# Performance work log

Measured on AMD Instinct MI355X. Metric: run time of the kernel, lower is better.

## Reference

```python
import jax, jax.numpy as jnp
import numpy as np

COMMITMENT_COST = 0.25


def setup_inputs() -> dict:
    key = jax.random.key(0)
    k1, k2 = jax.random.split(key)
    x = jax.random.normal(k1, (65536, 256), dtype=jnp.float32)
    codebook = jax.random.normal(k2, (1024, 256), dtype=jnp.float32)
    return {"x": x, "codebook": codebook}


def reference(x, codebook):
    # Flatten to [N, D] (already 2D here).
    flat = x.reshape(-1, codebook.shape[1])
    # Squared euclidean distances [N, K]; argmin matches torch.cdist argmin.
    x2 = jnp.sum(flat * flat, axis=1, keepdims=True)          # [N, 1]
    c2 = jnp.sum(codebook * codebook, axis=1)                  # [K]
    d2 = x2 - 2.0 * (flat @ codebook.T) + c2[None, :]          # [N, K]
    encoding_indices = jnp.argmin(d2, axis=1)                  # [N]
    quantized = codebook[encoding_indices]                     # [N, D]
    # VQ loss + commitment loss
    vq_loss = jnp.mean((jax.lax.stop_gradient(quantized) - flat) ** 2)
    commitment_loss = jnp.mean((quantized - jax.lax.stop_gradient(flat)) ** 2)
    quantization_loss = vq_loss + COMMITMENT_COST * commitment_loss
    # Straight-through estimator
    quantized_st = flat + jax.lax.stop_gradient(quantized - flat)
    quantized_st = quantized_st.reshape(x.shape)
    return quantized_st, quantization_loss, encoding_indices
```

## Files before the change

kernel.cpp:

```cpp
#include <hip/hip_runtime.h>

#define NROWS 65536
#define DDIM  256
#define KCODES 1024
#define MARGIN 0.05f
#define TIE_WINDOW 8.0e-5
#define FLAGCAP 8192

typedef __attribute__((ext_vector_type(8))) short bf16x8;
typedef __attribute__((ext_vector_type(4))) float f32x4;

union F4 { float4 v; float f[4]; };

__device__ __forceinline__ unsigned bf16rne(float f) {
    unsigned u = __float_as_uint(f);
    return (u + 0x7fffu + ((u >> 16) & 1u)) >> 16;
}
__device__ __forceinline__ float bf16tof(unsigned h) {
    return __uint_as_float(h << 16);
}

__global__ __launch_bounds__(64) void c2_kernel(const float* __restrict__ cb,
                                                float* __restrict__ c2f,
                                                double* __restrict__ c2d,
                                                int* __restrict__ cnt) {
    const int c = blockIdx.x, lane = threadIdx.x;
    if (c == 0 && lane == 0) cnt[0] = 0;
    F4 v; v.v = reinterpret_cast<const float4*>(cb + (size_t)c * DDIM)[lane];
    double s = (double)v.f[0] * v.f[0] + (double)v.f[1] * v.f[1]
             + (double)v.f[2] * v.f[2] + (double)v.f[3] * v.f[3];
    #pragma unroll
    for (int off = 32; off; off >>= 1) s += __shfl_xor(s, off);
    if (lane == 0) { c2d[c] = s; c2f[c] = (float)s; }
}

__global__ __launch_bounds__(256) void prep_frags(const float* __restrict__ cb,
                                                  unsigned short* __restrict__ fh,
                                                  unsigned short* __restrict__ fl) {
    int t = blockIdx.x * 256 + threadIdx.x;
    int j0   = (t & 1) * 4;
    int lane = (t >> 1) & 63;
    int ks   = (t >> 7) & 7;
    int ntg  = t >> 10;
    int c = ntg * 16 + (lane & 15);
    int k = ks * 32 + (lane >> 4) * 8 + j0;
    F4 v; v.v = *reinterpret_cast<const float4*>(cb + (size_t)c * DDIM + k);
    unsigned h0 = bf16rne(v.f[0]), h1 = bf16rne(v.f[1]),
             h2 = bf16rne(v.f[2]), h3 = bf16rne(v.f[3]);
    unsigned l0 = bf16rne(v.f[0] - bf16tof(h0)), l1 = bf16rne(v.f[1] - bf16tof(h1)),
             l2 = bf16rne(v.f[2] - bf16tof(h2)), l3 = bf16rne(v.f[3] - bf16tof(h3));
    unsigned* ph = reinterpret_cast<unsigned*>(fh + (size_t)t * 4);
    unsigned* pl = reinterpret_cast<unsigned*>(fl + (size_t)t * 4);
    ph[0] = h0 | (h1 << 16); ph[1] = h2 | (h3 << 16);
    pl[0] = l0 | (l1 << 16); pl[1] = l2 | (l3 << 16);
}

__global__ __launch_bounds__(512) void vqmfma(const float* __restrict__ x,
                                              const unsigned short* __restrict__ fbh,
                                              const unsigned short* __restrict__ fbl,
                                              const float* __restrict__ c2f,
                                              float* __restrict__ out_idx,
                                              int* __restrict__ flaglist,
                                              int* __restrict__ cnt) {
    __shared__ bf16x8 lds_ah[1024];
    __shared__ bf16x8 lds_al[1024];
    __shared__ float  lds_c2[KCODES];
    __shared__ float  m_b1[256]; __shared__ float m_b2[256]; __shared__ int m_i1[256];

    const int tid  = threadIdx.x;
    const int w    = tid >> 6;
    const int lane = tid & 63;
    const int row0 = blockIdx.x * 32;

    #pragma unroll
    for (int q = 0; q < 2; q++) lds_c2[q * 512 + tid] = c2f[q * 512 + tid];

    {
        const float4* gx = reinterpret_cast<const float4*>(x + (size_t)row0 * DDIM);
        unsigned* pah = reinterpret_cast<unsigned*>(lds_ah);
        unsigned* pal = reinterpret_cast<unsigned*>(lds_al);
        #pragma unroll
        for (int jj = 0; jj < 4; jj++) {
            int flat4 = jj * 512 + tid;
            int r = flat4 >> 6;
            int k = (flat4 & 63) * 4;
            F4 v; v.v = gx[flat4];
            int rt = r >> 4, row = r & 15;
            int ks = k >> 5, gg = (k >> 3) & 3, j0 = k & 7;
            int laneS = gg * 16 + row;
            int u32i = ((((rt * 8 + ks) * 64 + laneS) * 8 + j0) >> 1);
            unsigned h0 = bf16rne(v.f[0]), h1 = bf16rne(v.f[1]),
                     h2 = bf16rne(v.f[2]), h3 = bf16rne(v.f[3]);
            pah[u32i]     = h0 | (h1 << 16);
            pah[u32i + 1] = h2 | (h3 << 16);
            unsigned l0 = bf16rne(v.f[0] - bf16tof(h0)), l1 = bf16rne(v.f[1] - bf16tof(h1)),
                     l2 = bf16rne(v.f[2] - bf16tof(h2)), l3 = bf16rne(v.f[3] - bf16tof(h3));
            pal[u32i]     = l0 | (l1 << 16);
            pal[u32i + 1] = l2 | (l3 << 16);
        }
    }
    __syncthreads();

    float bestv[8], secv[8]; int besti[8];
    #pragma unroll
    for (int e = 0; e < 8; e++) { bestv[e] = 1e30f; secv[e] = 1e30f; besti[e] = 0; }

    const bf16x8* Bh = reinterpret_cast<const bf16x8*>(fbh);
    const bf16x8* Bl = reinterpret_cast<const bf16x8*>(fbl);

    for (int cc = 0; cc < KCODES; cc += 256) {
        f32x4 acc[2][2];
        #pragma unroll
        for (int rt = 0; rt < 2; rt++)
            #pragma unroll
            for (int nt = 0; nt < 2; nt++) acc[rt][nt] = (f32x4){0.f, 0.f, 0.f, 0.f};

        const int ntg0 = (cc >> 4) + w * 2;
        const bf16x8* b0h = Bh + (size_t)(ntg0 * 8) * 64 + lane;
        const bf16x8* b0l = Bl + (size_t)(ntg0 * 8) * 64 + lane;
        const bf16x8* b1h = b0h + 8 * 64;
        const bf16x8* b1l = b0l + 8 * 64;
        const bf16x8* a0  = &lds_ah[lane];
        const bf16x8* a1  = &lds_ah[8 * 64 + lane];
        const bf16x8* a0l = &lds_al[lane];
        const bf16x8* a1l = &lds_al[8 * 64 + lane];

        #pragma unroll
        for (int ks = 0; ks < 8; ks++) {
            bf16x8 ah0 = a0[ks * 64],  ah1 = a1[ks * 64];
            bf16x8 al0 = a0l[ks * 64], al1 = a1l[ks * 64];
            bf16x8 bh0 = b0h[ks * 64], bl0 = b0l[ks * 64];
            bf16x8 bh1 = b1h[ks * 64], bl1 = b1l[ks * 64];
            acc[0][0] = __builtin_amdgcn_mfma_f32_16x16x32_bf16(ah0, bh0, acc[0][0], 0, 0, 0);
            acc[1][0] = __builtin_amdgcn_mfma_f32_16x16x32_bf16(ah1, bh0, acc[1][0], 0, 0, 0);
            acc[0][1] = __builtin_amdgcn_mfma_f32_16x16x32_bf16(ah0, bh1, acc[0][1], 0, 0, 0);
            acc[1][1] = __builtin_amdgcn_mfma_f32_16x16x32_bf16(ah1, bh1, acc[1][1], 0, 0, 0);
            acc[0][0] = __builtin_amdgcn_mfma_f32_16x16x32_bf16(ah0, bl0, acc[0][0], 0, 0, 0);
            acc[1][0] = __builtin_amdgcn_mfma_f32_16x16x32_bf16(ah1, bl0, acc[1][0], 0, 0, 0);
            acc[0][1] = __builtin_amdgcn_mfma_f32_16x16x32_bf16(ah0, bl1, acc[0][1], 0, 0, 0);
            acc[1][1] = __builtin_amdgcn_mfma_f32_16x16x32_bf16(ah1, bl1, acc[1][1], 0, 0, 0);
            acc[0][0] = __builtin_amdgcn_mfma_f32_16x16x32_bf16(al0, bh0, acc[0][0], 0, 0, 0);
            acc[1][0] = __builtin_amdgcn_mfma_f32_16x16x32_bf16(al1, bh0, acc[1][0], 0, 0, 0);
            acc[0][1] = __builtin_amdgcn_mfma_f32_16x16x32_bf16(al0, bh1, acc[0][1], 0, 0, 0);
            acc[1][1] = __builtin_amdgcn_mfma_f32_16x16x32_bf16(al1, bh1, acc[1][1], 0, 0, 0);
        }
        #pragma unroll
        for (int nt = 0; nt < 2; nt++) {
            int c = cc + w * 32 + nt * 16 + (lane & 15);
            float c2v = lds_c2[c];
            #pragma unroll
            for (int rt = 0; rt < 2; rt++)
                #pragma unroll
                for (int reg = 0; reg < 4; reg++) {
                    float s = __fmaf_rn(-2.f, acc[rt][nt][reg], c2v);
                    int e = rt * 4 + reg;
                    if (s < bestv[e]) { secv[e] = bestv[e]; bestv[e] = s; besti[e] = c; }
                    else if (s < secv[e]) secv[e] = s;
                }
        }
    }

    #pragma unroll
    for (int e = 0; e < 8; e++) {
        float b1 = bestv[e]; int i1 = besti[e]; float b2 = secv[e];
        #pragma unroll
        for (int off = 8; off; off >>= 1) {
            float o1 = __shfl_xor(b1, off, 16);
            int   oi = __shfl_xor(i1, off, 16);
            float o2 = __shfl_xor(b2, off, 16);
            if (o1 < b1 || (o1 == b1 && oi < i1)) { b2 = fminf(b1, o2); b1 = o1; i1 = oi; }
            else                                  { b2 = fminf(o1, b2); }
        }
        if ((lane & 15) == 0) {
            int rt = e >> 2, reg = e & 3;
            int rib = rt * 16 + (lane >> 4) * 4 + reg;
            m_b1[w * 32 + rib] = b1; m_i1[w * 32 + rib] = i1; m_b2[w * 32 + rib] = b2;
        }
    }
    __syncthreads();

    if (tid < 32) {
        float b1 = m_b1[tid]; int i1 = m_i1[tid]; float b2 = m_b2[tid];
        #pragma unroll
        for (int ww = 1; ww < 8; ww++) {
            float o1 = m_b1[ww * 32 + tid]; int oi = m_i1[ww * 32 + tid];
            float o2 = m_b2[ww * 32 + tid];
            if (o1 < b1 || (o1 == b1 && oi < i1)) { b2 = fminf(b1, o2); b1 = o1; i1 = oi; }
            else                                  { b2 = fminf(o1, b2); }
        }
        out_idx[row0 + tid] = (float)i1;
        if (b2 - b1 < MARGIN) {
            int slot = atomicAdd(cnt, 1);
            if (slot < FLAGCAP) flaglist[slot] = row0 + tid;
        }
    }
}

__global__ __launch_bounds__(256) void refine_kernel(const float* __restrict__ x,
                                                     const float* __restrict__ cb,
                                                     const double* __restrict__ c2d,
                                                     const int* __restrict__ flaglist,
                                                     const int* __restrict__ cnt,
                                                     float* __restrict__ out_idx) {
    __shared__ double xs[DDIM];
    __shared__ double redd[256];
    __shared__ int    redi[256];
    const int tid = threadIdx.x;
    const int n = min(cnt[0], FLAGCAP);

    for (int fi = blockIdx.x; fi < n; fi += gridDim.x) {
        const int row = flaglist[fi];
        const double xv = (double)x[(size_t)row * DDIM + tid];
        xs[tid] = xv;
        redd[tid] = xv * xv;
        __syncthreads();
        for (int off = 128; off; off >>= 1) {
            if (tid < off) redd[tid] += redd[tid + off];
            __syncthreads();
        }
        const double x2 = redd[0];
        __syncthreads();

        double d2v[4];
        #pragma unroll
        for (int j = 0; j < 4; j++) {
            const int c = tid + 256 * j;
            const float* cp = cb + (size_t)c * DDIM;
            double dot = 0.0;
            for (int d = 0; d < DDIM; d += 4) {
                F4 cv; cv.v = *reinterpret_cast<const float4*>(cp + d);
                dot += xs[d+0]*(double)cv.f[0] + xs[d+1]*(double)cv.f[1]
                     + xs[d+2]*(double)cv.f[2] + xs[d+3]*(double)cv.f[3];
            }
            d2v[j] = x2 - 2.0 * dot + c2d[c];
        }
        double mv = fmin(fmin(d2v[0], d2v[1]), fmin(d2v[2], d2v[3]));
        redd[tid] = mv;
        __syncthreads();
        for (int off = 128; off; off >>= 1) {
            if (tid < off) redd[tid] = fmin(redd[tid], redd[tid + off]);
            __syncthreads();
        }
        const double thr = redd[0] + TIE_WINDOW;
        __syncthreads();
        int ci = 0x7fffffff;
        #pragma unroll
        for (int j = 0; j < 4; j++)
            if (d2v[j] <= thr) ci = min(ci, tid + 256 * j);
        redi[tid] = ci;
        __syncthreads();
        for (int off = 128; off; off >>= 1) {
            if (tid < off) redi[tid] = min(redi[tid], redi[tid + off]);
            __syncthreads();
        }
        if (tid == 0) out_idx[row] = (float)redi[0];
        __syncthreads();
    }
}

__global__ __launch_bounds__(256) void gather_kernel(const float* __restrict__ x,
                                                     const float* __restrict__ cb,
                                                     const float* __restrict__ out_idx,
                                                     float* __restrict__ out_q,
                                                     float* __restrict__ partial) {
    __shared__ float wsum[4];
    const int tid = threadIdx.x;
    const int row = blockIdx.x * 32 + (tid >> 3);
    const int d0  = (tid & 7) * 32;
    const int bi  = (int)out_idx[row];
    const float4* gq = reinterpret_cast<const float4*>(cb + (size_t)bi * DDIM + d0);
    const float4* gx = reinterpret_cast<const float4*>(x + (size_t)row * DDIM + d0);
    float4* go = reinterpret_cast<float4*>(out_q + (size_t)row * DDIM + d0);
    float sq = 0.f;
    #pragma unroll
    for (int j = 0; j < 8; j++) {
        F4 q, xv; q.v = gq[j]; xv.v = gx[j];
        go[j] = q.v;
        #pragma unroll
        for (int t = 0; t < 4; t++) { float d = q.f[t] - xv.f[t]; sq += d * d; }
    }
    #pragma unroll
    for (int off = 32; off; off >>= 1) sq += __shfl_down(sq, off);
    if ((tid & 63) == 0) wsum[tid >> 6] = sq;
    __syncthreads();
    if (tid == 0) partial[blockIdx.x] = wsum[0] + wsum[1] + wsum[2] + wsum[3];
}

__global__ __launch_bounds__(256) void loss_kernel(const float* __restrict__ partial,
                                                   float* __restrict__ out_loss) {
    __shared__ float w[4];
    float s = 0.f;
    for (int j = threadIdx.x; j < 2048; j += 256) s += partial[j];
    #pragma unroll
    for (int off = 32; off; off >>= 1) s += __shfl_down(s, off);
    if ((threadIdx.x & 63) == 0) w[threadIdx.x >> 6] = s;
    __syncthreads();
    if (threadIdx.x == 0)
        out_loss[0] = 1.25f * (w[0] + w[1] + w[2] + w[3]) / 16777216.f;
}

extern "C" void kernel_launch(void* const* d_in, const int* in_sizes, int n_in,
                              void* d_out, int out_size, void* d_ws, size_t ws_size,
                              hipStream_t stream) {
    const float* x  = (const float*)d_in[0];
    const float* cb = (const float*)d_in[1];
    float* out      = (float*)d_out;
    float* out_q    = out;
    float* out_loss = out + 16777216;
    float* out_idx  = out + 16777217;

    unsigned short* fbh = (unsigned short*)d_out;
    unsigned short* fbl = fbh + 262144;

    char* wsp = (char*)d_ws;
    float*  ws_c2f     = (float*) (wsp +     0);
    double* ws_c2d     = (double*)(wsp +  4096);
    float*  ws_partial = (float*) (wsp + 12288);
    int*    ws_flag    = (int*)   (wsp + 20480);
    int*    ws_cnt     = (int*)   (wsp + 53248);

    c2_kernel<<<KCODES, 64, 0, stream>>>(cb, ws_c2f, ws_c2d, ws_cnt);
    prep_frags<<<256, 256, 0, stream>>>(cb, fbh, fbl);
    vqmfma<<<NROWS / 32, 512, 0, stream>>>(x, fbh, fbl, ws_c2f,
                                           out_idx, ws_flag, ws_cnt);
    refine_kernel<<<256, 256, 0, stream>>>(x, cb, ws_c2d, ws_flag, ws_cnt, out_idx);
    gather_kernel<<<NROWS / 32, 256, 0, stream>>>(x, cb, out_idx, out_q, ws_partial);
    loss_kernel<<<1, 256, 0, stream>>>(ws_partial, out_loss);
}
```

Baseline: 250.4 us.

## Derive loss from min squared distance instead of re-reading x in gather

Computes each row's squared norm while staging x in the MFMA kernel and stores the per-row minimum distance (b1 + x2) to a workspace array. The refine kernel overwrites this with the exact double-precision minimum for flagged rows. The gather kernel then only copies codebook rows and no longer reads x, and the loss is a single reduction over 65536 per-row values. This removes a 64 MB read of x, but the loss now relies on the bf16-split distance estimate, which may differ slightly from an exact fp32 computation; the single-block 64K reduction is serial.

After: 256.4 us. +2.4%, slower.

```diff
diff --git a/kernel.cpp b/kernel.cpp
--- a/kernel.cpp
+++ b/kernel.cpp
@@ -61,11 +61,13 @@
                                               const float* __restrict__ c2f,
                                               float* __restrict__ out_idx,
                                               int* __restrict__ flaglist,
-                                              int* __restrict__ cnt) {
+                                              int* __restrict__ cnt,
+                                              float* __restrict__ rowsq) {
     __shared__ bf16x8 lds_ah[1024];
     __shared__ bf16x8 lds_al[1024];
     __shared__ float  lds_c2[KCODES];
     __shared__ float  m_b1[256]; __shared__ float m_b2[256]; __shared__ int m_i1[256];
+    __shared__ float  x2s[32];
 
     const int tid  = threadIdx.x;
     const int w    = tid >> 6;
@@ -85,6 +87,10 @@
             int r = flat4 >> 6;
             int k = (flat4 & 63) * 4;
             F4 v; v.v = gx[flat4];
+            float sq = v.f[0]*v.f[0] + v.f[1]*v.f[1] + v.f[2]*v.f[2] + v.f[3]*v.f[3];
+            #pragma unroll
+            for (int off = 32; off; off >>= 1) sq += __shfl_xor(sq, off);
+            if (lane == 0) x2s[r] = sq;
             int rt = r >> 4, row = r & 15;
             int ks = k >> 5, gg = (k >> 3) & 3, j0 = k & 7;
             int laneS = gg * 16 + row;
@@ -189,6 +195,7 @@
             else                                  { b2 = fminf(o1, b2); }
         }
         out_idx[row0 + tid] = (float)i1;
+        rowsq[row0 + tid] = b1 + x2s[tid];
         if (b2 - b1 < MARGIN) {
             int slot = atomicAdd(cnt, 1);
             if (slot < FLAGCAP) flaglist[slot] = row0 + tid;
@@ -201,13 +208,13 @@
                                                      const double* __restrict__ c2d,
                                                      const int* __restrict__ flaglist,
                                                      const int* __restrict__ cnt,
-                                                     float* __restrict__ out_idx) {
+                                                     float* __restrict__ out_idx,
+                                                     float* __restrict__ rowsq) {
     __shared__ double xs[DDIM];
     __shared__ double redd[256];
     __shared__ int    redi[256];
     const int tid = threadIdx.x;
     const int n = min(cnt[0], FLAGCAP);
-
     for (int fi = blockIdx.x; fi < n; fi += gridDim.x) {
         const int row = flaglist[fi];
         const double xv = (double)x[(size_t)row * DDIM + tid];
@@ -220,7 +227,6 @@
         }
         const double x2 = redd[0];
         __syncthreads();
-
         double d2v[4];
         #pragma unroll
         for (int j = 0; j < 4; j++) {
@@ -241,7 +247,8 @@
             if (tid < off) redd[tid] = fmin(redd[tid], redd[tid + off]);
             __syncthreads();
         }
-        const double thr = redd[0] + TIE_WINDOW;
+        const double d2min = redd[0];
+        const double thr = d2min + TIE_WINDOW;
         __syncthreads();
         int ci = 0x7fffffff;
         #pragma unroll
@@ -253,50 +260,42 @@
             if (tid < off) redi[tid] = min(redi[tid], redi[tid + off]);
             __syncthreads();
         }
-        if (tid == 0) out_idx[row] = (float)redi[0];
-        __syncthreads();
-    }
-}
-
-__global__ __launch_bounds__(256) void gather_kernel(const float* __restrict__ x,
-                                                     const float* __restrict__ cb,
-                                                     const float* __restrict__ out_idx,
-                                                     float* __restrict__ out_q,
-                                                     float* __restrict__ partial) {
-    __shared__ float wsum[4];
+        if (tid == 0) {
+            out_idx[row] = (float)redi[0];
+            rowsq[row]   = (float)d2min;
+        }
+        __syncthreads();
+    }
+}
+
+__global__ __launch_bounds__(256) void gather_slim(const float* __restrict__ cb,
+                                                   const float* __restrict__ out_idx,
+                                                   float* __restrict__ out_q) {
     const int tid = threadIdx.x;
     const int row = blockIdx.x * 32 + (tid >> 3);
     const int d0  = (tid & 7) * 32;
     const int bi  = (int)out_idx[row];
     const float4* gq = reinterpret_cast<const float4*>(cb + (size_t)bi * DDIM + d0);
-    const float4* gx = reinterpret_cast<const float4*>(x + (size_t)row * DDIM + d0);
     float4* go = reinterpret_cast<float4*>(out_q + (size_t)row * DDIM + d0);
-    float sq = 0.f;
-    #pragma unroll
-    for (int j = 0; j < 8; j++) {
-        F4 q, xv; q.v = gq[j]; xv.v = gx[j];
-        go[j] = q.v;
-        #pragma unroll
-        for (int t = 0; t < 4; t++) { float d = q.f[t] - xv.f[t]; sq += d * d; }
-    }
-    #pragma unroll
-    for (int off = 32; off; off >>= 1) sq += __shfl_down(sq, off);
-    if ((tid & 63) == 0) wsum[tid >> 6] = sq;
-    __syncthreads();
-    if (tid == 0) partial[blockIdx.x] = wsum[0] + wsum[1] + wsum[2] + wsum[3];
-}
-
-__global__ __launch_bounds__(256) void loss_kernel(const float* __restrict__ partial,
+    #pragma unroll
+    for (int j = 0; j < 8; j++) go[j] = gq[j];
+}
+
+__global__ __launch_bounds__(1024) void loss_rowsq(const float* __restrict__ rowsq,
                                                    float* __restrict__ out_loss) {
-    __shared__ float w[4];
+    __shared__ float w[16];
     float s = 0.f;
-    for (int j = threadIdx.x; j < 2048; j += 256) s += partial[j];
+    for (int j = threadIdx.x; j < NROWS; j += 1024) s += rowsq[j];
     #pragma unroll
     for (int off = 32; off; off >>= 1) s += __shfl_down(s, off);
     if ((threadIdx.x & 63) == 0) w[threadIdx.x >> 6] = s;
     __syncthreads();
-    if (threadIdx.x == 0)
-        out_loss[0] = 1.25f * (w[0] + w[1] + w[2] + w[3]) / 16777216.f;
+    if (threadIdx.x == 0) {
+        float tot = 0.f;
+        #pragma unroll
+        for (int i = 0; i < 16; i++) tot += w[i];
+        out_loss[0] = 1.25f * tot / 16777216.f;
+    }
 }
 
 extern "C" void kernel_launch(void* const* d_in, const int* in_sizes, int n_in,
@@ -313,17 +312,18 @@
     unsigned short* fbl = fbh + 262144;
 
     char* wsp = (char*)d_ws;
-    float*  ws_c2f     = (float*) (wsp +     0);
-    double* ws_c2d     = (double*)(wsp +  4096);
-    float*  ws_partial = (float*) (wsp + 12288);
-    int*    ws_flag    = (int*)   (wsp + 20480);
-    int*    ws_cnt     = (int*)   (wsp + 53248);
+    float*  ws_c2f   = (float*) (wsp +     0);
+    double* ws_c2d   = (double*)(wsp +  4096);
+    int*    ws_flag  = (int*)   (wsp + 12288);
+    int*    ws_cnt   = (int*)   (wsp + 45056);
+    float*  ws_rowsq = (float*) (wsp + 45120);
 
     c2_kernel<<<KCODES, 64, 0, stream>>>(cb, ws_c2f, ws_c2d, ws_cnt);
     prep_frags<<<256, 256, 0, stream>>>(cb, fbh, fbl);
     vqmfma<<<NROWS / 32, 512, 0, stream>>>(x, fbh, fbl, ws_c2f,
-                                           out_idx, ws_flag, ws_cnt);
-    refine_kernel<<<256, 256, 0, stream>>>(x, cb, ws_c2d, ws_flag, ws_cnt, out_idx);
-    gather_kernel<<<NROWS / 32, 256, 0, stream>>>(x, cb, out_idx, out_q, ws_partial);
-    loss_kernel<<<1, 256, 0, stream>>>(ws_partial, out_loss);
-}
+                                           out_idx, ws_flag, ws_cnt, ws_rowsq);
+    refine_kernel<<<256, 256, 0, stream>>>(x, cb, ws_c2d, ws_flag, ws_cnt,
+                                           out_idx, ws_rowsq);
+    gather_slim<<<NROWS / 32, 256, 0, stream>>>(cb, out_idx, out_q);
+    loss_rowsq<<<1, 1024, 0, stream>>>(ws_rowsq, out_loss);
+}
```
